# Kernel optimization log

Hardware: AMD Instinct MI355X
Metric: run time of the kernel (lower is better)

## Reference

```python
import jax, jax.numpy as jnp
import numpy as np

N_STATIONS = 100000
N_TIME = 1000
K_NEIGH = 8
SMOOTH = 0.2  # smoothing_factor


def setup_inputs() -> dict:
    key = jax.random.key(0)
    ks = jax.random.split(key, 7)
    time_vector = jax.random.uniform(ks[0], (N_TIME,), dtype=jnp.float32) * 5.0
    constant_offset = jax.random.normal(ks[1], (N_STATIONS,), dtype=jnp.float32)
    linear_trend = jax.random.normal(ks[2], (N_STATIONS,), dtype=jnp.float32)
    seasonal_amplitudes = jax.random.uniform(ks[3], (N_STATIONS, 4), dtype=jnp.float32) * 3.0
    seasonal_phases = jax.random.uniform(ks[4], (N_STATIONS, 4), dtype=jnp.float32) * (2.0 * np.pi)
    neighbor_indices = jax.random.randint(ks[5], (N_STATIONS, K_NEIGH), 0, N_STATIONS, dtype=jnp.int32)
    w = jax.random.uniform(ks[6], (N_STATIONS, K_NEIGH), dtype=jnp.float32) + 1e-3
    neighbor_weights = w / jnp.sum(w, axis=1, keepdims=True)  # row-normalized like the kNN weights
    periods = jnp.array([0.25, 0.5, 1.0, 2.0], dtype=jnp.float32)
    return {
        "time_vector": time_vector,
        "constant_offset": constant_offset,
        "linear_trend": linear_trend,
        "seasonal_amplitudes": seasonal_amplitudes,
        "seasonal_phases": seasonal_phases,
        "neighbor_indices": neighbor_indices,
        "neighbor_weights": neighbor_weights,
        "periods": periods,
    }


def _smooth_amp(amps, nbr_idx, nbr_w):
    # amps: [N,4], nbr_idx: [N,K], nbr_w: [N,K]
    nb = amps[nbr_idx]  # [N,K,4]
    avg = jnp.einsum('nkc,nk->nc', nb, nbr_w)
    return (1.0 - SMOOTH) * amps + SMOOTH * avg


def _smooth_phase(phases, nbr_idx, nbr_w):
    # circular-mean smoothing via unit complex vectors, done with real math
    nb = phases[nbr_idx]  # [N,K,4]
    avg_re = jnp.einsum('nkc,nk->nc', jnp.cos(nb), nbr_w)
    avg_im = jnp.einsum('nkc,nk->nc', jnp.sin(nb), nbr_w)
    mix_re = (1.0 - SMOOTH) * jnp.cos(phases) + SMOOTH * avg_re
    mix_im = (1.0 - SMOOTH) * jnp.sin(phases) + SMOOTH * avg_im
    return jnp.arctan2(mix_im, mix_re)


def reference(time_vector, constant_offset, linear_trend, seasonal_amplitudes,
              seasonal_phases, neighbor_indices, neighbor_weights, periods):
    amp_s = _smooth_amp(seasonal_amplitudes, neighbor_indices, neighbor_weights)   # [N,4]
    ph_s = _smooth_phase(seasonal_phases, neighbor_indices, neighbor_weights)      # [N,4]
    t = time_vector[None, :]  # [1,T]
    signals = constant_offset[:, None] + linear_trend[:, None] * t  # [N,T]
    two_pi = jnp.float32(2.0 * np.pi)
    for i in range(4):  # fixed small number of seasonal components
        freq = 1.0 / periods[i]
        signals = signals + amp_s[:, i:i+1] * jnp.sin(two_pi * freq * t + ph_s[:, i:i+1])
    return signals
```

## Files before the change

kernel.cpp:

```cpp
#include <hip/hip_runtime.h>
#include <math.h>

#define N_STATIONS 100000
#define N_TIME     1000
#define K_NEIGH    8
#define SPB        50

__global__ __launch_bounds__(256) void insar_kernel(
    const float* __restrict__ time_vector,
    const float* __restrict__ constant_offset,
    const float* __restrict__ linear_trend,
    const float* __restrict__ amps,
    const float* __restrict__ phases,
    const int*   __restrict__ nbr_idx,
    const float* __restrict__ nbr_w,
    const float* __restrict__ periods,
    float*       __restrict__ out)
{
    __shared__ float lds_cs[SPB * 4];
    __shared__ float lds_cc[SPB * 4];
    __shared__ float lds_off[SPB];
    __shared__ float lds_tr[SPB];

    const int tid = threadIdx.x;
    const int n0  = blockIdx.x * SPB;
    const float TWO_PI = 6.28318530717958647692f;

    float t4[4];
    float stab[4][4], ctab[4][4];
    if (tid < 250) {
        const float4 tv = *(const float4*)(time_vector + 4 * tid);
        t4[0] = tv.x; t4[1] = tv.y; t4[2] = tv.z; t4[3] = tv.w;
#pragma unroll
        for (int i = 0; i < 4; ++i) {
            const float w = TWO_PI / periods[i];
#pragma unroll
            for (int j = 0; j < 4; ++j) {
                sincosf(w * t4[j], &stab[i][j], &ctab[i][j]);
            }
        }
    }

    if (tid < SPB * 4) {
        const int s = tid >> 2;
        const int c = tid & 3;
        const int n = n0 + s;
        const float a0 = amps[n * 4 + c];
        const float p0 = phases[n * 4 + c];
        float accA = 0.f, accRe = 0.f, accIm = 0.f;
#pragma unroll
        for (int k = 0; k < K_NEIGH; ++k) {
            const int   idx = nbr_idx[n * 8 + k];
            const float w   = nbr_w[n * 8 + k];
            const float a   = amps[idx * 4 + c];
            const float p   = phases[idx * 4 + c];
            float sp, cp;
            sincosf(p, &sp, &cp);
            accA  = fmaf(w, a,  accA);
            accRe = fmaf(w, cp, accRe);
            accIm = fmaf(w, sp, accIm);
        }
        const float amp_s = 0.8f * a0 + 0.2f * accA;
        float s0, c0;
        sincosf(p0, &s0, &c0);
        const float mre = 0.8f * c0 + 0.2f * accRe;
        const float mim = 0.8f * s0 + 0.2f * accIm;
        const float r2  = mre * mre + mim * mim;
        float cs, cc;
        if (r2 > 1e-30f) {
            const float rinv = rsqrtf(r2);
            cs = amp_s * mre * rinv;
            cc = amp_s * mim * rinv;
        } else {
            cs = amp_s;
            cc = 0.f;
        }
        lds_cs[tid] = cs;
        lds_cc[tid] = cc;
    } else if (tid >= 200 && tid < 200 + SPB) {
        const int s = tid - 200;
        lds_off[s] = constant_offset[n0 + s];
        lds_tr[s]  = linear_trend[n0 + s];
    }
    __syncthreads();

    if (tid < 250) {
        for (int s = 0; s < SPB; ++s) {
            const int n   = n0 + s;
            const float off = lds_off[s];
            const float tr  = lds_tr[s];
            const float cS0 = lds_cs[s * 4 + 0], cS1 = lds_cs[s * 4 + 1];
            const float cS2 = lds_cs[s * 4 + 2], cS3 = lds_cs[s * 4 + 3];
            const float cC0 = lds_cc[s * 4 + 0], cC1 = lds_cc[s * 4 + 1];
            const float cC2 = lds_cc[s * 4 + 2], cC3 = lds_cc[s * 4 + 3];
            float4 o;
            float* op = &o.x;
#pragma unroll
            for (int j = 0; j < 4; ++j) {
                float v = fmaf(tr, t4[j], off);
                v = fmaf(cS0, stab[0][j], v);
                v = fmaf(cC0, ctab[0][j], v);
                v = fmaf(cS1, stab[1][j], v);
                v = fmaf(cC1, ctab[1][j], v);
                v = fmaf(cS2, stab[2][j], v);
                v = fmaf(cC2, ctab[2][j], v);
                v = fmaf(cS3, stab[3][j], v);
                v = fmaf(cC3, ctab[3][j], v);
                op[j] = v;
            }
            *(float4*)(out + (size_t)n * N_TIME + 4 * tid) = o;
        }
    }
}

extern "C" void kernel_launch(void* const* d_in, const int* in_sizes, int n_in,
                              void* d_out, int out_size, void* d_ws, size_t ws_size,
                              hipStream_t stream) {
    const float* time_vector     = (const float*)d_in[0];
    const float* constant_offset = (const float*)d_in[1];
    const float* linear_trend    = (const float*)d_in[2];
    const float* amps            = (const float*)d_in[3];
    const float* phases          = (const float*)d_in[4];
    const int*   nbr_idx         = (const int*)  d_in[5];
    const float* nbr_w           = (const float*)d_in[6];
    const float* periods         = (const float*)d_in[7];
    float* out = (float*)d_out;

    dim3 grid(N_STATIONS / SPB);
    insar_kernel<<<grid, 256, 0, stream>>>(time_vector, constant_offset, linear_trend,
                                           amps, phases, nbr_idx, nbr_w, periods, out);
}
```

Measured before the change: 488.4 us.

## Split into time-table, coefficient, and streaming store kernels via workspace

Splits the fused kernel into three launches. One precomputes the sin/cos time tables once, one computes the per-station smoothed coefficients at full occupancy into a workspace record, and one streams the output using those precomputed values. The aim is to take the gather, transcendental and barrier work off the store-bound main kernel, so each block no longer idles while the neighbour gather finishes. In exchange it adds two extra launches and a global-memory round trip for the coefficients and tables.

```diff
diff --git a/kernel.cpp b/kernel.cpp
--- a/kernel.cpp
+++ b/kernel.cpp
@@ -6,110 +6,134 @@
 #define K_NEIGH    8
 #define SPB        50
 
-__global__ __launch_bounds__(256) void insar_kernel(
+#define TTAB_PLANE   N_TIME
+#define REC_OFF      8192
+#define REC_STRIDE   16
+
+__global__ __launch_bounds__(256) void ttab_kernel(
     const float* __restrict__ time_vector,
+    const float* __restrict__ periods,
+    float*       __restrict__ ws)
+{
+    const int tid = threadIdx.x;
+    if (tid >= 250) return;
+    const float TWO_PI = 6.28318530717958647692f;
+    const float4 tv = *(const float4*)(time_vector + 4 * tid);
+    float t4[4] = { tv.x, tv.y, tv.z, tv.w };
+#pragma unroll
+    for (int i = 0; i < 4; ++i) {
+        const float w = TWO_PI / periods[i];
+        float4 s4, c4;
+        float* sp = &s4.x;
+        float* cp = &c4.x;
+#pragma unroll
+        for (int j = 0; j < 4; ++j) sincosf(w * t4[j], &sp[j], &cp[j]);
+        *(float4*)(ws + (2 * i)     * TTAB_PLANE + 4 * tid) = s4;
+        *(float4*)(ws + (2 * i + 1) * TTAB_PLANE + 4 * tid) = c4;
+    }
+}
+
+__global__ __launch_bounds__(256) void coef_kernel(
     const float* __restrict__ constant_offset,
     const float* __restrict__ linear_trend,
     const float* __restrict__ amps,
     const float* __restrict__ phases,
     const int*   __restrict__ nbr_idx,
     const float* __restrict__ nbr_w,
-    const float* __restrict__ periods,
+    float*       __restrict__ ws)
+{
+    const int g = blockIdx.x * 256 + threadIdx.x;
+    if (g >= N_STATIONS * 4) return;
+    const int n = g >> 2;
+    const int c = g & 3;
+
+    const float a0 = amps[g];
+    const float p0 = phases[g];
+
+    float accA = 0.f, accRe = 0.f, accIm = 0.f;
+#pragma unroll
+    for (int k = 0; k < K_NEIGH; ++k) {
+        const int   idx = nbr_idx[n * 8 + k];
+        const float w   = nbr_w[n * 8 + k];
+        const float a   = amps[idx * 4 + c];
+        const float p   = phases[idx * 4 + c];
+        float sp, cp;
+        sincosf(p, &sp, &cp);
+        accA  = fmaf(w, a,  accA);
+        accRe = fmaf(w, cp, accRe);
+        accIm = fmaf(w, sp, accIm);
+    }
+    const float amp_s = 0.8f * a0 + 0.2f * accA;
+    float s0, c0;
+    sincosf(p0, &s0, &c0);
+    const float mre = 0.8f * c0 + 0.2f * accRe;
+    const float mim = 0.8f * s0 + 0.2f * accIm;
+    const float r2  = mre * mre + mim * mim;
+    float cs, cc;
+    if (r2 > 1e-30f) {
+        const float rinv = rsqrtf(r2);
+        cs = amp_s * mre * rinv;
+        cc = amp_s * mim * rinv;
+    } else {
+        cs = amp_s;
+        cc = 0.f;
+    }
+    float* rec = ws + REC_OFF + (size_t)n * REC_STRIDE;
+    rec[c]     = cs;
+    rec[4 + c] = cc;
+    if (c == 0) {
+        rec[8] = constant_offset[n];
+        rec[9] = linear_trend[n];
+    }
+}
+
+__global__ __launch_bounds__(256) void insar_main(
+    const float* __restrict__ time_vector,
+    const float* __restrict__ ws,
     float*       __restrict__ out)
 {
-    __shared__ float lds_cs[SPB * 4];
-    __shared__ float lds_cc[SPB * 4];
-    __shared__ float lds_off[SPB];
-    __shared__ float lds_tr[SPB];
+    const int tid = threadIdx.x;
+    if (tid >= 250) return;
+    const int n0 = blockIdx.x * SPB;
 
-    const int tid = threadIdx.x;
-    const int n0  = blockIdx.x * SPB;
-    const float TWO_PI = 6.28318530717958647692f;
+    const float4 tv = *(const float4*)(time_vector + 4 * tid);
+    float t4[4] = { tv.x, tv.y, tv.z, tv.w };
 
-    float t4[4];
-    float stab[4][4], ctab[4][4];
-    if (tid < 250) {
-        const float4 tv = *(const float4*)(time_vector + 4 * tid);
-        t4[0] = tv.x; t4[1] = tv.y; t4[2] = tv.z; t4[3] = tv.w;
+    float st[4][4], ct[4][4];
 #pragma unroll
-        for (int i = 0; i < 4; ++i) {
-            const float w = TWO_PI / periods[i];
-#pragma unroll
-            for (int j = 0; j < 4; ++j) {
-                sincosf(w * t4[j], &stab[i][j], &ctab[i][j]);
-            }
-        }
+    for (int i = 0; i < 4; ++i) {
+        const float4 s4 = *(const float4*)(ws + (2 * i)     * TTAB_PLANE + 4 * tid);
+        const float4 c4 = *(const float4*)(ws + (2 * i + 1) * TTAB_PLANE + 4 * tid);
+        st[i][0] = s4.x; st[i][1] = s4.y; st[i][2] = s4.z; st[i][3] = s4.w;
+        ct[i][0] = c4.x; ct[i][1] = c4.y; ct[i][2] = c4.z; ct[i][3] = c4.w;
     }
 
-    if (tid < SPB * 4) {
-        const int s = tid >> 2;
-        const int c = tid & 3;
-        const int n = n0 + s;
-        const float a0 = amps[n * 4 + c];
-        const float p0 = phases[n * 4 + c];
-        float accA = 0.f, accRe = 0.f, accIm = 0.f;
+    const float* rec0 = ws + REC_OFF + (size_t)n0 * REC_STRIDE;
+    float* orow = out + (size_t)n0 * N_TIME + 4 * tid;
+
+    for (int s = 0; s < SPB; ++s) {
+        const float* rec = rec0 + s * REC_STRIDE;
+        const float cs0 = rec[0], cs1 = rec[1], cs2 = rec[2], cs3 = rec[3];
+        const float cc0 = rec[4], cc1 = rec[5], cc2 = rec[6], cc3 = rec[7];
+        const float off = rec[8], tr = rec[9];
+
+        float4 o;
+        float* op = &o.x;
 #pragma unroll
-        for (int k = 0; k < K_NEIGH; ++k) {
-            const int   idx = nbr_idx[n * 8 + k];
-            const float w   = nbr_w[n * 8 + k];
-            const float a   = amps[idx * 4 + c];
-            const float p   = phases[idx * 4 + c];
-            float sp, cp;
-            sincosf(p, &sp, &cp);
-            accA  = fmaf(w, a,  accA);
-            accRe = fmaf(w, cp, accRe);
-            accIm = fmaf(w, sp, accIm);
+        for (int j = 0; j < 4; ++j) {
+            float v = fmaf(tr, t4[j], off);
+            v = fmaf(cs0, st[0][j], v);
+            v = fmaf(cc0, ct[0][j], v);
+            v = fmaf(cs1, st[1][j], v);
+            v = fmaf(cc1, ct[1][j], v);
+            v = fmaf(cs2, st[2][j], v);
+            v = fmaf(cc2, ct[2][j], v);
+            v = fmaf(cs3, st[3][j], v);
+            v = fmaf(cc3, ct[3][j], v);
+            op[j] = v;
         }
-        const float amp_s = 0.8f * a0 + 0.2f * accA;
-        float s0, c0;
-        sincosf(p0, &s0, &c0);
-        const float mre = 0.8f * c0 + 0.2f * accRe;
-        const float mim = 0.8f * s0 + 0.2f * accIm;
-        const float r2  = mre * mre + mim * mim;
-        float cs, cc;
-        if (r2 > 1e-30f) {
-            const float rinv = rsqrtf(r2);
-            cs = amp_s * mre * rinv;
-            cc = amp_s * mim * rinv;
-        } else {
-            cs = amp_s;
-            cc = 0.f;
-        }
-        lds_cs[tid] = cs;
-        lds_cc[tid] = cc;
-    } else if (tid >= 200 && tid < 200 + SPB) {
-        const int s = tid - 200;
-        lds_off[s] = constant_offset[n0 + s];
-        lds_tr[s]  = linear_trend[n0 + s];
-    }
-    __syncthreads();
-
-    if (tid < 250) {
-        for (int s = 0; s < SPB; ++s) {
-            const int n   = n0 + s;
-            const float off = lds_off[s];
-            const float tr  = lds_tr[s];
-            const float cS0 = lds_cs[s * 4 + 0], cS1 = lds_cs[s * 4 + 1];
-            const float cS2 = lds_cs[s * 4 + 2], cS3 = lds_cs[s * 4 + 3];
-            const float cC0 = lds_cc[s * 4 + 0], cC1 = lds_cc[s * 4 + 1];
-            const float cC2 = lds_cc[s * 4 + 2], cC3 = lds_cc[s * 4 + 3];
-            float4 o;
-            float* op = &o.x;
-#pragma unroll
-            for (int j = 0; j < 4; ++j) {
-                float v = fmaf(tr, t4[j], off);
-                v = fmaf(cS0, stab[0][j], v);
-                v = fmaf(cC0, ctab[0][j], v);
-                v = fmaf(cS1, stab[1][j], v);
-                v = fmaf(cC1, ctab[1][j], v);
-                v = fmaf(cS2, stab[2][j], v);
-                v = fmaf(cC2, ctab[2][j], v);
-                v = fmaf(cS3, stab[3][j], v);
-                v = fmaf(cC3, ctab[3][j], v);
-                op[j] = v;
-            }
-            *(float4*)(out + (size_t)n * N_TIME + 4 * tid) = o;
-        }
+        *(float4*)orow = o;
+        orow += N_TIME;
     }
 }
 
@@ -125,8 +149,11 @@
     const float* nbr_w           = (const float*)d_in[6];
     const float* periods         = (const float*)d_in[7];
     float* out = (float*)d_out;
+    float* ws  = (float*)d_ws;
 
-    dim3 grid(N_STATIONS / SPB);
-    insar_kernel<<<grid, 256, 0, stream>>>(time_vector, constant_offset, linear_trend,
-                                           amps, phases, nbr_idx, nbr_w, periods, out);
+    ttab_kernel<<<1, 256, 0, stream>>>(time_vector, periods, ws);
+    const int coef_blocks = (N_STATIONS * 4 + 255) / 256;
+    coef_kernel<<<coef_blocks, 256, 0, stream>>>(constant_offset, linear_trend,
+                                                 amps, phases, nbr_idx, nbr_w, ws);
+    insar_main<<<N_STATIONS / SPB, 256, 0, stream>>>(time_vector, ws, out);
 }
```

Result: faster. 451.6 us (-7.5%).
